# Kernel optimization log

Hardware: AMD Instinct MI355X
Metric: run time of the kernel (lower is better)

## Reference

```python
import jax, jax.numpy as jnp
import numpy as np

DIM = 1024
DIM_FEAT = 384
HIDDEN = 1024
HEADS = 16
D_HEAD = HIDDEN // HEADS
SCALE = D_HEAD ** -0.5
EPS = 1e-5


def _layernorm(x, g, b):
    mu = jnp.mean(x, axis=-1, keepdims=True)
    var = jnp.var(x, axis=-1, keepdims=True)
    return (x - mu) * jax.lax.rsqrt(var + EPS) * g + b


def _split_heads(t):
    b, n, _ = t.shape
    return t.reshape(b, n, HEADS, D_HEAD).transpose(0, 2, 1, 3)  # b h n d


def _merge_heads(t):
    b, h, n, d = t.shape
    return t.transpose(0, 2, 1, 3).reshape(b, n, h * d)


def _attn(q, k, v):
    dots = jnp.einsum('bhnd,bhmd->bhnm', q, k) * SCALE
    attn = jax.nn.softmax(dots, axis=-1)
    return jnp.einsum('bhnm,bhmd->bhnd', attn, v)


def setup_inputs() -> dict:
    key = jax.random.key(0)
    ks = jax.random.split(key, 10)
    B, N = 2, 2048
    s = lambda fan: 1.0 / np.sqrt(fan)
    return {
        'x': jax.random.normal(ks[0], (B, N, DIM), jnp.float32),
        'feature': jax.random.normal(ks[1], (B, N, DIM_FEAT), jnp.float32),
        'norm_g': jnp.ones((DIM,), jnp.float32),
        'norm_b': jnp.zeros((DIM,), jnp.float32),
        'W_cq': jax.random.normal(ks[2], (DIM, HIDDEN), jnp.float32) * s(DIM),
        'W_ckv': jax.random.normal(ks[3], (DIM_FEAT, 2 * HIDDEN), jnp.float32) * s(DIM_FEAT),
        'W_sqkv': jax.random.normal(ks[4], (DIM, 3 * HIDDEN), jnp.float32) * s(DIM),
        'ffn_g': jnp.ones((DIM,), jnp.float32),
        'ffn_b': jnp.zeros((DIM,), jnp.float32),
        'W1': jax.random.normal(ks[5], (DIM, 4 * DIM), jnp.float32) * s(DIM),
        'b1': jnp.zeros((4 * DIM,), jnp.float32),
        'W2': jax.random.normal(ks[6], (4 * DIM, DIM), jnp.float32) * s(4 * DIM),
        'b2': jnp.zeros((DIM,), jnp.float32),
    }


def reference(x, feature, norm_g, norm_b, W_cq, W_ckv, W_sqkv, ffn_g, ffn_b, W1, b1, W2, b2):
    # cross attention
    xn = _layernorm(x, norm_g, norm_b)
    q = _split_heads(xn @ W_cq)
    kv = feature @ W_ckv
    k, v = jnp.split(kv, 2, axis=-1)
    cross = _merge_heads(_attn(q, _split_heads(k), _split_heads(v))) + x
    # self attention (shared norm)
    cn = _layernorm(cross, norm_g, norm_b)
    qkv = cn @ W_sqkv
    sq, sk, sv = (_split_heads(t) for t in jnp.split(qkv, 3, axis=-1))
    self_tok = _merge_heads(_attn(sq, sk, sv)) + cross
    # FFN with its own layernorm
    h = _layernorm(self_tok, ffn_g, ffn_b)
    h = jax.nn.gelu(h @ W1 + b1, approximate=False)
    out = h @ W2 + b2
    return out + self_tok
```

## Files before the change

kernel.cpp:

```cpp
#include <hip/hip_runtime.h>
#include <math.h>
#include <stdint.h>

typedef __attribute__((ext_vector_type(8)))  short   short8;
typedef __attribute__((ext_vector_type(4)))  short   short4v;
typedef __attribute__((ext_vector_type(8)))  __bf16  bf16x8;
typedef __attribute__((ext_vector_type(4)))  float   f32x4;
typedef __attribute__((ext_vector_type(16))) float   f32x16;

__device__ __forceinline__ unsigned short f2b(float f) {
    union { float f; unsigned u; } v; v.f = f;
    unsigned r = v.u + 0x7FFF + ((v.u >> 16) & 1);
    return (unsigned short)(r >> 16);
}

__device__ __forceinline__ f32x4 mfma_bf16(bf16x8 a, bf16x8 b, f32x4 c) {
    return __builtin_amdgcn_mfma_f32_16x16x32_bf16(a, b, c, 0, 0, 0);
}

__device__ __forceinline__ f32x16 mfma32(bf16x8 a, bf16x8 b, f32x16 c) {
    return __builtin_amdgcn_mfma_f32_32x32x16_bf16(a, b, c, 0, 0, 0);
}

__device__ __forceinline__ unsigned cvt_pk_bf16(float lo, float hi) {
    unsigned r;
    asm volatile("v_cvt_pk_bf16_f32 %0, %1, %2" : "=v"(r) : "v"(lo), "v"(hi));
    return r;
}

__device__ __forceinline__ void gload_lds16(const unsigned short* g, unsigned short* l) {
    __builtin_amdgcn_global_load_lds(
        (const __attribute__((address_space(1))) void*)g,
        (__attribute__((address_space(3))) void*)l,
        16, 0, 0);
}

template <int N>
__device__ __forceinline__ void wait_vmcnt() {
    if constexpr (N == 0)       asm volatile("s_waitcnt vmcnt(0)" ::: "memory");
    else if constexpr (N == 4)  asm volatile("s_waitcnt vmcnt(4)" ::: "memory");
    else if constexpr (N == 6)  asm volatile("s_waitcnt vmcnt(6)" ::: "memory");
    else if constexpr (N == 8)  asm volatile("s_waitcnt vmcnt(8)" ::: "memory");
    else                        static_assert(N == 0 || N == 4 || N == 6 || N == 8, "add vmcnt case");
}

#define QSCALE 0.18033688011112042592f

__global__ __launch_bounds__(256) void wconv_t(const float* __restrict__ W,
                                               unsigned short* __restrict__ Wt,
                                               int K, int N) {
    __shared__ float tile[32][33];
    int bk = blockIdx.x * 32;
    int bn = blockIdx.y * 32;
    int tx = threadIdx.x & 31, ty = threadIdx.x >> 5;
#pragma unroll
    for (int i = 0; i < 4; ++i) {
        int r = ty + i * 8;
        tile[r][tx] = W[(size_t)(bk + r) * N + bn + tx];
    }
    __syncthreads();
#pragma unroll
    for (int i = 0; i < 4; ++i) {
        int r = ty + i * 8;
        Wt[(size_t)(bn + r) * K + bk + tx] = f2b(tile[tx][r]);
    }
}

__global__ __launch_bounds__(256) void fconv(const float* __restrict__ in,
                                             unsigned short* __restrict__ out, int n4) {
    int i = blockIdx.x * 256 + threadIdx.x;
    if (i >= n4) return;
    f32x4 v = ((const f32x4*)in)[i];
    short4v o;
    o.x = (short)f2b(v.x); o.y = (short)f2b(v.y);
    o.z = (short)f2b(v.z); o.w = (short)f2b(v.w);
    ((short4v*)out)[i] = o;
}

__global__ __launch_bounds__(256) void lnorm(const float* __restrict__ x,
                                             const float* __restrict__ g,
                                             const float* __restrict__ bta,
                                             unsigned short* __restrict__ out) {
    int row = blockIdx.x;
    const f32x4* xr = (const f32x4*)(x + (size_t)row * 1024);
    int t = threadIdx.x;
    f32x4 v = xr[t];
    float s  = v.x + v.y + v.z + v.w;
    float s2 = v.x * v.x + v.y * v.y + v.z * v.z + v.w * v.w;
#pragma unroll
    for (int m = 1; m < 64; m <<= 1) {
        s  += __shfl_xor(s, m);
        s2 += __shfl_xor(s2, m);
    }
    __shared__ float rs[8];
    int w = t >> 6;
    if ((t & 63) == 0) { rs[w] = s; rs[4 + w] = s2; }
    __syncthreads();
    s  = rs[0] + rs[1] + rs[2] + rs[3];
    s2 = rs[4] + rs[5] + rs[6] + rs[7];
    float mean = s * (1.0f / 1024.0f);
    float var  = s2 * (1.0f / 1024.0f) - mean * mean;
    float rstd = rsqrtf(var + 1e-5f);
    f32x4 gv = ((const f32x4*)g)[t];
    f32x4 bv = ((const f32x4*)bta)[t];
    short4v o;
    o.x = (short)f2b((v.x - mean) * rstd * gv.x + bv.x);
    o.y = (short)f2b((v.y - mean) * rstd * gv.y + bv.y);
    o.z = (short)f2b((v.z - mean) * rstd * gv.z + bv.z);
    o.w = (short)f2b((v.w - mean) * rstd * gv.w + bv.w);
    ((short4v*)(out + (size_t)row * 1024))[t] = o;
}

template <int WM, int WN, int MI, int NI, int EPI, bool SCQ>
__global__ __launch_bounds__(WM * WN * 64, 2)
void gemm8(const unsigned short* __restrict__ A,
           const unsigned short* __restrict__ Bt,
           void* __restrict__ C,
           const float* __restrict__ bias,
           const float* __restrict__ resid,
           int M, int N, int K, int scale_cols) {
    constexpr int BM = WM * MI * 16;
    constexpr int BN = WN * NI * 16;
    constexpr int THREADS = WM * WN * 64;
    constexpr int ROWS = THREADS / 8;
    constexpr int IA = BM / ROWS;
    constexpr int IB = BN / ROWS;

    const int nwg = gridDim.x;
    const int nby = N / BN;
    int flat = blockIdx.x;
    int wk = (flat & 7) * (nwg >> 3) + (flat >> 3);
    const int m0 = (wk / nby) * BM;
    const int n0 = (wk % nby) * BN;

    __shared__ unsigned short As[2][BM * 64];
    __shared__ unsigned short Bs[2][BN * 64];

    const int tid  = threadIdx.x;
    const int lane = tid & 63;
    const int wid  = tid >> 6;
    const int wm = wid / WN, wn = wid % WN;
    const int l15 = lane & 15, q4 = lane >> 4, xw = lane & 7;

    const int sr = tid >> 3;
    const int sg = (tid & 7) ^ (sr & 7);

    const unsigned short* ag = A  + (size_t)(m0 + sr) * K + sg * 8;
    const unsigned short* bg = Bt + (size_t)(n0 + sr) * K + sg * 8;

    f32x4 acc[MI][NI] = {};

    auto STAGE = [&](int d, int t) {
        const int k0 = t * 64;
#pragma unroll
        for (int i = 0; i < IA; ++i)
            gload_lds16(ag + (size_t)(i * ROWS) * K + k0, &As[d][i * ROWS * 64 + tid * 8]);
#pragma unroll
        for (int i = 0; i < IB; ++i)
            gload_lds16(bg + (size_t)(i * ROWS) * K + k0, &Bs[d][i * ROWS * 64 + tid * 8]);
    };

    const int NT = K >> 6;
    STAGE(0, 0);

    for (int t = 0; t < NT; ++t) {
        const int c = t & 1;
        if (t + 1 < NT) STAGE(c ^ 1, t + 1);
        __builtin_amdgcn_sched_barrier(0);
        if (t + 1 < NT) wait_vmcnt<IA + IB>();
        else            wait_vmcnt<0>();
        __builtin_amdgcn_s_barrier();
        __builtin_amdgcn_sched_barrier(0);
#pragma unroll
        for (int h = 0; h < 2; ++h) {
            bf16x8 a[MI], b[NI];
            const int gsl = h * 4 + q4;
#pragma unroll
            for (int mi = 0; mi < MI; ++mi)
                a[mi] = *(const bf16x8*)&As[c][(wm * MI * 16 + mi * 16 + l15) * 64 + ((gsl ^ xw) << 3)];
#pragma unroll
            for (int ni = 0; ni < NI; ++ni)
                b[ni] = *(const bf16x8*)&Bs[c][(wn * NI * 16 + ni * 16 + l15) * 64 + ((gsl ^ xw) << 3)];
            __builtin_amdgcn_s_setprio(1);
#pragma unroll
            for (int mi = 0; mi < MI; ++mi)
#pragma unroll
                for (int ni = 0; ni < NI; ++ni)
                    acc[mi][ni] = mfma_bf16(a[mi], b[ni], acc[mi][ni]);
            __builtin_amdgcn_s_setprio(0);
        }
        __builtin_amdgcn_sched_barrier(0);
        __builtin_amdgcn_s_barrier();
    }

    const int rb = m0 + wm * MI * 16 + q4 * 4;
    const int cb = n0 + wn * NI * 16 + l15;
    float bv[NI];
    if (EPI >= 1) {
#pragma unroll
        for (int ni = 0; ni < NI; ++ni) bv[ni] = bias[cb + ni * 16];
    }
#pragma unroll
    for (int mi = 0; mi < MI; ++mi) {
#pragma unroll
        for (int r = 0; r < 4; ++r) {
            const int row = rb + mi * 16 + r;
#pragma unroll
            for (int ni = 0; ni < NI; ++ni) {
                const int col = cb + ni * 16;
                float v = acc[mi][ni][r];
                if (EPI == 0) {
                    if (SCQ && col < scale_cols) v *= QSCALE;
                    ((unsigned short*)C)[(size_t)row * N + col] = f2b(v);
                } else if (EPI == 1) {
                    v += bv[ni];
                    v = 0.5f * v * (1.0f + erff(v * 0.70710678118f));
                    ((unsigned short*)C)[(size_t)row * N + col] = f2b(v);
                } else {
                    v += bv[ni] + resid[(size_t)row * N + col];
                    ((float*)C)[(size_t)row * N + col] = v;
                }
            }
        }
    }
}

template <int EPI, bool SCQ>
__global__ __launch_bounds__(512, 2)
void gemm256(const unsigned short* __restrict__ A,
             const unsigned short* __restrict__ Bt,
             void* __restrict__ C,
             const float* __restrict__ bias,
             const float* __restrict__ resid,
             int M, int N, int K, int scale_cols) {
    const int nby = N / 256;
    const int nwg = gridDim.x;
    int flat = blockIdx.x;
    int wk = (flat & 7) * (nwg >> 3) + (flat >> 3);
    const int m0 = (wk / nby) * 256;
    const int n0 = (wk % nby) * 256;

    __shared__ unsigned short As[2][256 * 64];
    __shared__ unsigned short Bs[2][256 * 64];

    const int tid  = threadIdx.x;
    const int lane = tid & 63;
    const int wid  = tid >> 6;
    const int wm = wid >> 2, wn = wid & 3;
    const int l15 = lane & 15, q4 = lane >> 4, xw = lane & 7;

    const int sr = tid >> 3;
    const int sg = (tid & 7) ^ (sr & 7);

    const unsigned short* ag = A  + (size_t)(m0 + sr) * K + sg * 8;
    const unsigned short* bg = Bt + (size_t)(n0 + sr) * K + sg * 8;

    f32x4 acc[8][4] = {};

#define SA256(d, t, i) gload_lds16(ag + (size_t)((i) * 64) * K + (t) * 64, &As[d][(i) * 4096 + tid * 8])
#define SB256(d, t, i) gload_lds16(bg + (size_t)((i) * 64) * K + (t) * 64, &Bs[d][(i) * 4096 + tid * 8])

    const int NT = K >> 6;
#pragma unroll
    for (int i = 0; i < 4; ++i) { SA256(0, 0, i); SB256(0, 0, i); }
    wait_vmcnt<0>();
    __builtin_amdgcn_s_barrier();

    for (int t = 0; t < NT; ++t) {
        const int c = t & 1;
        const bool pf = (t + 1 < NT);
        bf16x8 breg[4];
#pragma unroll
        for (int p = 0; p < 4; ++p) {
            const int h = p >> 1, mh = p & 1;
            const int col = ((h * 4 + q4) ^ xw) << 3;
            if ((p & 1) == 0) {
#pragma unroll
                for (int ni = 0; ni < 4; ++ni)
                    breg[ni] = *(const bf16x8*)&Bs[c][(wn * 64 + ni * 16 + l15) * 64 + col];
            }
            bf16x8 a[4];
#pragma unroll
            for (int mi = 0; mi < 4; ++mi)
                a[mi] = *(const bf16x8*)&As[c][(wm * 128 + mh * 64 + mi * 16 + l15) * 64 + col];
            if (pf) {
                if (p == 0)      { SA256(c ^ 1, t + 1, 0); SB256(c ^ 1, t + 1, 0); SA256(c ^ 1, t + 1, 1); }
                else if (p == 1) { SB256(c ^ 1, t + 1, 1); SA256(c ^ 1, t + 1, 2); SB256(c ^ 1, t + 1, 2); }
                else if (p == 2) { SA256(c ^ 1, t + 1, 3); SB256(c ^ 1, t + 1, 3); }
            }
            __builtin_amdgcn_sched_barrier(0);
            asm volatile("s_waitcnt lgkmcnt(0)" ::: "memory");
            __builtin_amdgcn_sched_barrier(0);
            __builtin_amdgcn_s_setprio(1);
#pragma unroll
            for (int mi = 0; mi < 4; ++mi)
#pragma unroll
                for (int ni = 0; ni < 4; ++ni)
                    acc[mh * 4 + mi][ni] = mfma_bf16(a[mi], breg[ni], acc[mh * 4 + mi][ni]);
            __builtin_amdgcn_s_setprio(0);
            __builtin_amdgcn_sched_barrier(0);
            if (p == 3) wait_vmcnt<0>();
            __builtin_amdgcn_s_barrier();
        }
    }
#undef SA256
#undef SB256

    const int rb = m0 + wm * 128 + q4 * 4;
    const int cb = n0 + wn * 64 + l15;
    float bv[4];
    if (EPI >= 1) {
#pragma unroll
        for (int ni = 0; ni < 4; ++ni) bv[ni] = bias[cb + ni * 16];
    }
#pragma unroll
    for (int ai = 0; ai < 8; ++ai) {
#pragma unroll
        for (int r = 0; r < 4; ++r) {
            const int row = rb + ai * 16 + r;
#pragma unroll
            for (int ni = 0; ni < 4; ++ni) {
                const int col = cb + ni * 16;
                float v = acc[ai][ni][r];
                if (EPI == 0) {
                    if (SCQ && col < scale_cols) v *= QSCALE;
                    ((unsigned short*)C)[(size_t)row * N + col] = f2b(v);
                } else if (EPI == 1) {
                    v += bv[ni];
                    v = 0.5f * v * (1.0f + erff(v * 0.70710678118f));
                    ((unsigned short*)C)[(size_t)row * N + col] = f2b(v);
                } else {
                    v += bv[ni] + resid[(size_t)row * N + col];
                    ((float*)C)[(size_t)row * N + col] = v;
                }
            }
        }
    }
}

__global__ __launch_bounds__(256) void kvpack(const unsigned short* __restrict__ src,
                                              int stride, int k_off, int v_off,
                                              unsigned short* __restrict__ pack) {
    const int oct = blockIdx.x;
    const int bh  = blockIdx.y;
    const int b = bh >> 4, h = bh & 15;
    const int tid = threadIdx.x;
    const int lane = tid & 63;
    const int sl = tid >> 6;
    const int l31 = lane & 31, l5 = lane >> 5;
    __shared__ unsigned short Kl[32 * 64], Vl[32 * 64];
    const int r = tid >> 3, c8 = (tid & 7) * 8;
    for (int t8 = 0; t8 < 8; ++t8) {
        const int kt = oct * 8 + t8;
        const int kb = kt * 32;
        *(short8*)&Kl[r * 64 + c8] = *(const short8*)&src[(size_t)(b * 2048 + kb + r) * stride + k_off + h * 64 + c8];
        *(short8*)&Vl[r * 64 + c8] = *(const short8*)&src[(size_t)(b * 2048 + kb + r) * stride + v_off + h * 64 + c8];
        __syncthreads();
        unsigned short* o = pack + (size_t)bh * 262144 + (size_t)kt * 4096;
        *(short8*)&o[sl * 512 + lane * 8] = *(const short8*)&Kl[l31 * 64 + sl * 16 + l5 * 8];
        {
            const int dh = sl >> 1, c2 = sl & 1;
            short8 vv;
#pragma unroll
            for (int j = 0; j < 8; ++j)
                vv[j] = (short)Vl[(c2 * 16 + l5 * 8 + j) * 64 + dh * 32 + l31];
            *(short8*)&o[(4 + sl) * 512 + lane * 8] = vv;
        }
        __syncthreads();
    }
}

__global__ __launch_bounds__(256) void attn(const unsigned short* __restrict__ Q, int q_stride, int q_off,
                                            const unsigned short* __restrict__ pack,
                                            const float* __restrict__ res,
                                            float* __restrict__ out) {
    const int bid = blockIdx.x;
    const int slot = bid >> 3;
    const int bh = (bid & 7) * 4 + (slot >> 5);
    const int qt = slot & 31;
    const int b = bh >> 4, h = bh & 15;
    const int tid = threadIdx.x;
    const int lane = tid & 63, w = tid >> 6;
    const int qg = w >> 1, ks = w & 1;
    const int l31 = lane & 31, l5 = lane >> 5;

    __shared__ unsigned short lds[2][8192];

    const int q0 = qt * 64 + qg * 32;

    const unsigned short* qp = Q + (size_t)(b * 2048 + q0 + l31) * q_stride + q_off + h * 64 + l5 * 8;
    bf16x8 qf[4];
#pragma unroll
    for (int i = 0; i < 4; ++i) qf[i] = *(const bf16x8*)&qp[i * 16];

    const unsigned short* pkb = pack + (size_t)bh * 262144;

    f32x16 oacc[2] = {};
    f32x16 lacc = {};

    auto STAGE = [&](int d, int t) {
        const unsigned short* s = pkb + (size_t)t * 8192;
#pragma unroll
        for (int i = 0; i < 4; ++i) {
            const int ch = i * 4 + w;
            gload_lds16(s + ch * 512 + lane * 8, &lds[d][ch * 512 + lane * 8]);
        }
    };

    STAGE(0, 0);

    for (int t = 0; t < 32; ++t) {
        const int cur = t & 1;
        if (t + 1 < 32) STAGE(cur ^ 1, t + 1);
        __builtin_amdgcn_sched_barrier(0);
        if (t + 1 < 32) wait_vmcnt<4>();
        else            wait_vmcnt<0>();
        __builtin_amdgcn_s_barrier();
        __builtin_amdgcn_sched_barrier(0);

        const unsigned short* L = &lds[cur][ks * 4096 + lane * 8];

        bf16x8 kf[4];
#pragma unroll
        for (int i = 0; i < 4; ++i) kf[i] = *(const bf16x8*)&L[i * 512];

        f32x16 s = {};
        __builtin_amdgcn_s_setprio(1);
#pragma unroll
        for (int i = 0; i < 4; ++i) s = mfma32(kf[i], qf[i], s);
        __builtin_amdgcn_s_setprio(0);

        bf16x8 vf[2][2];
#pragma unroll
        for (int dh = 0; dh < 2; ++dh)
#pragma unroll
            for (int c2 = 0; c2 < 2; ++c2)
                vf[dh][c2] = *(const bf16x8*)&L[(4 + dh * 2 + c2) * 512];

        float p[16];
#pragma unroll
        for (int r = 0; r < 16; ++r) p[r] = __builtin_amdgcn_exp2f(s[r]);
#pragma unroll
        for (int r = 0; r < 16; ++r) lacc[r] += p[r];

        bf16x8 pf[2];
#pragma unroll
        for (int c = 0; c < 2; ++c) {
            unsigned a0 = cvt_pk_bf16(p[8 * c + 0], p[8 * c + 1]);
            unsigned a1 = cvt_pk_bf16(p[8 * c + 4], p[8 * c + 5]);
            unsigned b0 = cvt_pk_bf16(p[8 * c + 2], p[8 * c + 3]);
            unsigned b1 = cvt_pk_bf16(p[8 * c + 6], p[8 * c + 7]);
            asm volatile("v_permlane32_swap_b32 %0, %1" : "+v"(a0), "+v"(a1));
            asm volatile("v_permlane32_swap_b32 %0, %1" : "+v"(b0), "+v"(b1));
            union { unsigned u[4]; bf16x8 v; } pu;
            pu.u[0] = a0; pu.u[1] = b0; pu.u[2] = a1; pu.u[3] = b1;
            pf[c] = pu.v;
        }

        __builtin_amdgcn_s_setprio(1);
#pragma unroll
        for (int dh = 0; dh < 2; ++dh)
#pragma unroll
            for (int c2 = 0; c2 < 2; ++c2)
                oacc[dh] = mfma32(vf[dh][c2], pf[c2], oacc[dh]);
        __builtin_amdgcn_s_setprio(0);

        __builtin_amdgcn_s_barrier();
    }

    float lsum[16];
#pragma unroll
    for (int r = 0; r < 16; ++r) lsum[r] = lacc[r];
#pragma unroll
    for (int off = 8; off >= 1; off >>= 1)
#pragma unroll
        for (int r = 0; r < off; ++r) lsum[r] += lsum[r + off];
    float lh = lsum[0] + __shfl_xor(lsum[0], 32);

    float* mb = (float*)&lds[qg][0];
    if (ks == 1) {
#pragma unroll
        for (int dh = 0; dh < 2; ++dh)
#pragma unroll
            for (int r = 0; r < 16; ++r)
                mb[lane * 33 + dh * 16 + r] = oacc[dh][r];
        mb[lane * 33 + 32] = lh;
    }
    __syncthreads();
    if (ks == 0) {
#pragma unroll
        for (int dh = 0; dh < 2; ++dh)
#pragma unroll
            for (int r = 0; r < 16; ++r)
                oacc[dh][r] += mb[lane * 33 + dh * 16 + r];
        const float l = lh + mb[lane * 33 + 32];

        const float inv = 1.0f / l;
        const size_t rowoff = (size_t)(b * 2048 + q0 + l31) * 1024 + h * 64;
#pragma unroll
        for (int dh = 0; dh < 2; ++dh) {
#pragma unroll
            for (int g = 0; g < 4; ++g) {
                const int col = dh * 32 + g * 8 + l5 * 4;
                f32x4 rv = *(const f32x4*)&res[rowoff + col];
                f32x4 ov;
#pragma unroll
                for (int r = 0; r < 4; ++r) ov[r] = oacc[dh][g * 4 + r] * inv + rv[r];
                *(f32x4*)&out[rowoff + col] = ov;
            }
        }
    }
}

extern "C" void kernel_launch(void* const* d_in, const int* in_sizes, int n_in,
                              void* d_out, int out_size, void* d_ws, size_t ws_size,
                              hipStream_t stream) {
    const float* x      = (const float*)d_in[0];
    const float* feat   = (const float*)d_in[1];
    const float* norm_g = (const float*)d_in[2];
    const float* norm_b = (const float*)d_in[3];
    const float* W_cq   = (const float*)d_in[4];
    const float* W_ckv  = (const float*)d_in[5];
    const float* W_sqkv = (const float*)d_in[6];
    const float* ffn_g  = (const float*)d_in[7];
    const float* ffn_b  = (const float*)d_in[8];
    const float* W1     = (const float*)d_in[9];
    const float* b1     = (const float*)d_in[10];
    const float* W2     = (const float*)d_in[11];
    const float* b2     = (const float*)d_in[12];
    float* out = (float*)d_out;

    char* ws = (char*)d_ws;
    unsigned short* wq_t   = (unsigned short*)(ws + (size_t)(0u)   * (1u << 20));
    unsigned short* wkv_t  = (unsigned short*)(ws + (size_t)(2u)   * (1u << 20));
    unsigned short* wqkv_t = (unsigned short*)(ws + (size_t)(4u)   * (1u << 20));
    unsigned short* w1_t   = (unsigned short*)(ws + (size_t)(10u)  * (1u << 20));
    unsigned short* w2_t   = (unsigned short*)(ws + (size_t)(18u)  * (1u << 20));
    unsigned short* featb  = (unsigned short*)(ws + (size_t)(26u)  * (1u << 20));
    unsigned short* t0     = (unsigned short*)(ws + (size_t)(29u)  * (1u << 20));
    float*          cross  = (float*)        (ws + (size_t)(37u)  * (1u << 20));
    unsigned short* qb     = (unsigned short*)(ws + (size_t)(53u)  * (1u << 20));
    unsigned short* kvb    = (unsigned short*)(ws + (size_t)(61u)  * (1u << 20));
    unsigned short* qkvb   = (unsigned short*)(ws + (size_t)(77u)  * (1u << 20));
    unsigned short* packb  = (unsigned short*)(ws + (size_t)(101u) * (1u << 20));
    unsigned short* h1     = (unsigned short*)(ws + (size_t)(53u)  * (1u << 20));

    wconv_t<<<dim3(1024 / 32, 1024 / 32), 256, 0, stream>>>(W_cq,   wq_t,   1024, 1024);
    wconv_t<<<dim3(384 / 32,  2048 / 32), 256, 0, stream>>>(W_ckv,  wkv_t,  384,  2048);
    wconv_t<<<dim3(1024 / 32, 3072 / 32), 256, 0, stream>>>(W_sqkv, wqkv_t, 1024, 3072);
    wconv_t<<<dim3(1024 / 32, 4096 / 32), 256, 0, stream>>>(W1,     w1_t,   1024, 4096);
    wconv_t<<<dim3(4096 / 32, 1024 / 32), 256, 0, stream>>>(W2,     w2_t,   4096, 1024);
    fconv<<<dim3((4096 * 384 / 4) / 256), 256, 0, stream>>>(feat, featb, 4096 * 384 / 4);

    lnorm<<<4096, 256, 0, stream>>>(x, norm_g, norm_b, t0);
    gemm8<2, 2, 4, 2, 0, true ><<<512, 256, 0, stream>>>(t0,    wq_t,  qb,  nullptr, nullptr, 4096, 1024, 1024, 1024);
    gemm8<2, 2, 4, 4, 0, false><<<512, 256, 0, stream>>>(featb, wkv_t, kvb, nullptr, nullptr, 4096, 2048, 384,  0);
    kvpack<<<dim3(8, 32), 256, 0, stream>>>(kvb, 2048, 0, 1024, packb);
    attn<<<1024, 256, 0, stream>>>(qb, 1024, 0, packb, x, cross);

    lnorm<<<4096, 256, 0, stream>>>(cross, norm_g, norm_b, t0);
    gemm256<0, true ><<<192, 512, 0, stream>>>(t0, wqkv_t, qkvb, nullptr, nullptr, 4096, 3072, 1024, 1024);
    kvpack<<<dim3(8, 32), 256, 0, stream>>>(qkvb, 3072, 1024, 2048, packb);
    attn<<<1024, 256, 0, stream>>>(qkvb, 3072, 0, packb, cross, out);

    lnorm<<<4096, 256, 0, stream>>>(out, ffn_g, ffn_b, t0);
    gemm256<1, false><<<256, 512, 0, stream>>>(t0, w1_t, h1, b1, nullptr, 4096, 4096, 1024, 0);
    gemm8<2, 2, 4, 2, 2, false><<<512, 256, 0, stream>>>(h1, w2_t, out, b2, (const float*)out, 4096, 1024, 4096, 0);
}
```

Baseline: 329.5 us.

## Split-K the FFN down-projection with 256-tile GEMM and bf16 partial merge

The W2 GEMM (4096x1024, K=4096) moves from the smaller gemm8 kernel to the 256x256 gemm256 kernel with a 4-way K split, giving 256 workgroups. Each split writes bf16 partial sums to workspace. A new kmerge kernel adds the four partials, the bias and the residual already held in the output. This targets the low tile count and poor occupancy of the down-projection, at the cost of extra partial-sum traffic, an additional launch, and bf16 rounding of the partial sums.

Result: faster. 321.4 us (-2.5%).

```diff
diff --git a/kernel.cpp b/kernel.cpp
--- a/kernel.cpp
+++ b/kernel.cpp
@@ -12,6 +12,10 @@
     union { float f; unsigned u; } v; v.f = f;
     unsigned r = v.u + 0x7FFF + ((v.u >> 16) & 1);
     return (unsigned short)(r >> 16);
+}
+
+__device__ __forceinline__ float b2f(unsigned short u) {
+    union { unsigned u; float f; } v; v.u = (unsigned)u << 16; return v.f;
 }
 
 __device__ __forceinline__ f32x4 mfma_bf16(bf16x8 a, bf16x8 b, f32x4 c) {
@@ -225,20 +229,25 @@
     }
 }
 
-template <int EPI, bool SCQ>
+template <int EPI, bool SCQ, int KSPLIT>
 __global__ __launch_bounds__(512, 2)
 void gemm256(const unsigned short* __restrict__ A,
              const unsigned short* __restrict__ Bt,
              void* __restrict__ C,
              const float* __restrict__ bias,
-             const float* __restrict__ resid,
-             int M, int N, int K, int scale_cols) {
+             unsigned short* __restrict__ ph0,
+             unsigned short* __restrict__ ph1,
+             int M, int N, int lda, int ldb, int klen, int scale_cols) {
     const int nby = N / 256;
+    const int nmn = (M / 256) * nby;
     const int nwg = gridDim.x;
     int flat = blockIdx.x;
     int wk = (flat & 7) * (nwg >> 3) + (flat >> 3);
+    int ks = 0;
+    if constexpr (KSPLIT > 1) { ks = wk / nmn; wk -= ks * nmn; }
     const int m0 = (wk / nby) * 256;
     const int n0 = (wk % nby) * 256;
+    const int koff = ks * klen;
 
     __shared__ unsigned short As[2][256 * 64];
     __shared__ unsigned short Bs[2][256 * 64];
@@ -252,15 +261,15 @@
     const int sr = tid >> 3;
     const int sg = (tid & 7) ^ (sr & 7);
 
-    const unsigned short* ag = A  + (size_t)(m0 + sr) * K + sg * 8;
-    const unsigned short* bg = Bt + (size_t)(n0 + sr) * K + sg * 8;
+    const unsigned short* ag = A  + (size_t)(m0 + sr) * lda + koff + sg * 8;
+    const unsigned short* bg = Bt + (size_t)(n0 + sr) * ldb + koff + sg * 8;
 
     f32x4 acc[8][4] = {};
 
-#define SA256(d, t, i) gload_lds16(ag + (size_t)((i) * 64) * K + (t) * 64, &As[d][(i) * 4096 + tid * 8])
-#define SB256(d, t, i) gload_lds16(bg + (size_t)((i) * 64) * K + (t) * 64, &Bs[d][(i) * 4096 + tid * 8])
-
-    const int NT = K >> 6;
+#define SA256(d, t, i) gload_lds16(ag + (size_t)((i) * 64) * lda + (t) * 64, &As[d][(i) * 4096 + tid * 8])
+#define SB256(d, t, i) gload_lds16(bg + (size_t)((i) * 64) * ldb + (t) * 64, &Bs[d][(i) * 4096 + tid * 8])
+
+    const int NT = klen >> 6;
 #pragma unroll
     for (int i = 0; i < 4; ++i) { SA256(0, 0, i); SB256(0, 0, i); }
     wait_vmcnt<0>();
@@ -309,10 +318,12 @@
     const int rb = m0 + wm * 128 + q4 * 4;
     const int cb = n0 + wn * 64 + l15;
     float bv[4];
-    if (EPI >= 1) {
+    if (EPI == 1) {
 #pragma unroll
         for (int ni = 0; ni < 4; ++ni) bv[ni] = bias[cb + ni * 16];
     }
+    unsigned short* pb = nullptr;
+    if (EPI == 3) pb = ((ks & 2) ? ph1 : ph0) + (size_t)(ks & 1) * ((size_t)M * N);
 #pragma unroll
     for (int ai = 0; ai < 8; ++ai) {
 #pragma unroll
@@ -330,12 +341,34 @@
                     v = 0.5f * v * (1.0f + erff(v * 0.70710678118f));
                     ((unsigned short*)C)[(size_t)row * N + col] = f2b(v);
                 } else {
-                    v += bv[ni] + resid[(size_t)row * N + col];
-                    ((float*)C)[(size_t)row * N + col] = v;
+                    pb[(size_t)row * N + col] = f2b(v);
                 }
             }
         }
     }
+}
+
+__global__ __launch_bounds__(256) void kmerge(const unsigned short* __restrict__ p01,
+                                              const unsigned short* __restrict__ p23,
+                                              const float* __restrict__ bias,
+                                              float* __restrict__ out) {
+    const size_t i4 = (size_t)blockIdx.x * 256 + threadIdx.x;
+    const size_t e = i4 * 4;
+    const int col4 = (int)(e & 1023);
+    f32x4 acc = *(const f32x4*)&bias[col4];
+    const size_t MN = (size_t)4096 * 1024;
+#pragma unroll
+    for (int k = 0; k < 2; ++k) {
+        short4v a = *(const short4v*)&p01[k * MN + e];
+        short4v b = *(const short4v*)&p23[k * MN + e];
+        acc.x += b2f((unsigned short)a.x) + b2f((unsigned short)b.x);
+        acc.y += b2f((unsigned short)a.y) + b2f((unsigned short)b.y);
+        acc.z += b2f((unsigned short)a.z) + b2f((unsigned short)b.z);
+        acc.w += b2f((unsigned short)a.w) + b2f((unsigned short)b.w);
+    }
+    f32x4 o = *(const f32x4*)&out[e];
+    o.x += acc.x; o.y += acc.y; o.z += acc.z; o.w += acc.w;
+    *(f32x4*)&out[e] = o;
 }
 
 __global__ __launch_bounds__(256) void kvpack(const unsigned short* __restrict__ src,
@@ -544,6 +577,8 @@
     unsigned short* qkvb   = (unsigned short*)(ws + (size_t)(77u)  * (1u << 20));
     unsigned short* packb  = (unsigned short*)(ws + (size_t)(101u) * (1u << 20));
     unsigned short* h1     = (unsigned short*)(ws + (size_t)(53u)  * (1u << 20));
+    unsigned short* part01 = (unsigned short*)(ws + (size_t)(37u)  * (1u << 20));
+    unsigned short* part23 = (unsigned short*)(ws + (size_t)(101u) * (1u << 20));
 
     wconv_t<<<dim3(1024 / 32, 1024 / 32), 256, 0, stream>>>(W_cq,   wq_t,   1024, 1024);
     wconv_t<<<dim3(384 / 32,  2048 / 32), 256, 0, stream>>>(W_ckv,  wkv_t,  384,  2048);
@@ -559,11 +594,12 @@
     attn<<<1024, 256, 0, stream>>>(qb, 1024, 0, packb, x, cross);
 
     lnorm<<<4096, 256, 0, stream>>>(cross, norm_g, norm_b, t0);
-    gemm256<0, true ><<<192, 512, 0, stream>>>(t0, wqkv_t, qkvb, nullptr, nullptr, 4096, 3072, 1024, 1024);
+    gemm256<0, true , 1><<<192, 512, 0, stream>>>(t0, wqkv_t, qkvb, nullptr, nullptr, nullptr, 4096, 3072, 1024, 1024, 1024, 1024);
     kvpack<<<dim3(8, 32), 256, 0, stream>>>(qkvb, 3072, 1024, 2048, packb);
     attn<<<1024, 256, 0, stream>>>(qkvb, 3072, 0, packb, cross, out);
 
     lnorm<<<4096, 256, 0, stream>>>(out, ffn_g, ffn_b, t0);
-    gemm256<1, false><<<256, 512, 0, stream>>>(t0, w1_t, h1, b1, nullptr, 4096, 4096, 1024, 0);
-    gemm8<2, 2, 4, 2, 2, false><<<512, 256, 0, stream>>>(h1, w2_t, out, b2, (const float*)out, 4096, 1024, 4096, 0);
-}
+    gemm256<1, false, 1><<<256, 512, 0, stream>>>(t0, w1_t, h1, b1, nullptr, nullptr, 4096, 4096, 1024, 1024, 1024, 0);
+    gemm256<3, false, 4><<<256, 512, 0, stream>>>(h1, w2_t, nullptr, nullptr, part01, part23, 4096, 1024, 4096, 4096, 1024, 0);
+    kmerge<<<4096, 256, 0, stream>>>(part01, part23, b2, out);
+}
```
